# Kernel optimization log

Measured on AMD Instinct MI355X. Metric: run time of the kernel, lower is better.

## Reference

```python
import jax, jax.numpy as jnp
import numpy as np

B = 4096
SEQ = 128            # window_size * rnn_in_pkts
WINDOW = 32
IN_PKTS = 4
LEN_V, LEN_E = 1500, 64
IPD_V, IPD_E = 256, 64
EV = 64              # embedding_vector_bits
RNN_IN = IN_PKTS * EV   # 256
H = 256              # rnn_hidden_bits
LABELS = 100


def setup_inputs() -> dict:
    key = jax.random.key(0)
    ks = jax.random.split(key, 12)
    s = 0.05
    return {
        "len_x": jax.random.randint(ks[0], (B, SEQ), 0, LEN_V),
        "ipd_x": jax.random.randint(ks[1], (B, SEQ), 0, IPD_V),
        "len_emb": jax.random.normal(ks[2], (LEN_V, LEN_E), jnp.float32) * s,
        "ipd_emb": jax.random.normal(ks[3], (IPD_V, IPD_E), jnp.float32) * s,
        "fc_w": jax.random.normal(ks[4], (EV, LEN_E + IPD_E), jnp.float32) * s,
        "fc_b": jax.random.normal(ks[5], (EV,), jnp.float32) * s,
        "w_ih": jax.random.normal(ks[6], (3 * H, RNN_IN), jnp.float32) * s,
        "w_hh": jax.random.normal(ks[7], (3 * H, H), jnp.float32) * s,
        "b_ih": jax.random.normal(ks[8], (3 * H,), jnp.float32) * s,
        "b_hh": jax.random.normal(ks[9], (3 * H,), jnp.float32) * s,
        "out_w": jax.random.normal(ks[10], (LABELS, H), jnp.float32) * s,
        "out_b": jax.random.normal(ks[11], (LABELS,), jnp.float32) * s,
    }


def _gru_scan(rnn_in, w_ih, w_hh, b_ih, b_hh):
    # rnn_in: [B, T, RNN_IN]. Precompute input-side gates for all steps at once.
    gi_all = jnp.einsum("bti,gi->btg", rnn_in, w_ih) + b_ih  # [B,T,3H]
    h0 = jnp.zeros((rnn_in.shape[0], H), rnn_in.dtype)

    def step(h, gi):
        gh = h @ w_hh.T + b_hh                 # [B,3H]
        i_r, i_z, i_n = jnp.split(gi, 3, axis=-1)
        h_r, h_z, h_n = jnp.split(gh, 3, axis=-1)
        r = jax.nn.sigmoid(i_r + h_r)
        z = jax.nn.sigmoid(i_z + h_z)
        n = jnp.tanh(i_n + r * h_n)
        h_new = (1.0 - z) * n + z * h
        return h_new, None

    h_final, _ = jax.lax.scan(step, h0, jnp.swapaxes(gi_all, 0, 1))
    return h_final


def reference(len_x, ipd_x, len_emb, ipd_emb, fc_w, fc_b, w_ih, w_hh, b_ih, b_hh, out_w, out_b):
    len_e = len_emb[len_x]                      # [B,SEQ,LEN_E]
    ipd_e = ipd_emb[ipd_x]                      # [B,SEQ,IPD_E]
    cat = jnp.concatenate([len_e, ipd_e], axis=-1)
    evs = cat @ fc_w.T + fc_b                   # [B,SEQ,EV]
    rnn_in = evs.reshape(B, WINDOW, RNN_IN)     # [B,32,256]
    h = _gru_scan(rnn_in, w_ih, w_hh, b_ih, b_hh)
    logits = h @ out_w.T + out_b                # [B,LABELS]
    return logits
```

## Files before the change

### kernel.cpp

```cpp
#include <hip/hip_runtime.h>
#include <hip/hip_bf16.h>

typedef __bf16 bf16_t;
typedef __bf16 bf16x8 __attribute__((ext_vector_type(8)));
typedef float f32x4 __attribute__((ext_vector_type(4)));
typedef unsigned short u16x4 __attribute__((ext_vector_type(4)));

#define MFMA16(a, b, c) __builtin_amdgcn_mfma_f32_16x16x32_bf16((a), (b), (c), 0, 0, 0)

#define BATCH 4096
#define SEQN 128
#define HN 256
#define NLABELS 100
#define TSTEPS 32
#define LEN_VN 1500
#define IPD_VN 256

#define OFF_LENT   0u
#define OFF_IPDT   384000u
#define OFF_WIH    449536u
#define OFF_WHH    842752u
#define OFF_GI     1235968u

__device__ __forceinline__ float sigf(float x) {
    return __builtin_amdgcn_rcpf(1.f + __expf(-x));
}
__device__ __forceinline__ float tanh_fast(float x) {
    return 2.f * __builtin_amdgcn_rcpf(1.f + __expf(-2.f * x)) - 1.f;
}
__device__ __forceinline__ float b2f(unsigned short v) {
    union { unsigned u; float f; } c; c.u = ((unsigned)v) << 16; return c.f;
}
__device__ __forceinline__ f32x4 b2f4(u16x4 v) {
    f32x4 o;
    #pragma unroll
    for (int r = 0; r < 4; ++r) o[r] = b2f(v[r]);
    return o;
}
__device__ __forceinline__ unsigned short f2b(float f) {
    union { bf16_t h; unsigned short s; } c; c.h = (bf16_t)f; return c.s;
}

__device__ __forceinline__ void barrier_lds() {
    asm volatile("s_waitcnt lgkmcnt(0)\n\ts_barrier" ::: "memory");
}
__device__ __forceinline__ void wait_vm0() {
    asm volatile("s_waitcnt vmcnt(0)" ::: "memory");
}

#define PREP_TBL_BLOCKS 110
__global__ void prep_kernel(const float* __restrict__ len_emb,
                            const float* __restrict__ ipd_emb,
                            const float* __restrict__ fc_w,
                            const float* __restrict__ fc_b,
                            const float* __restrict__ w_ih,
                            const float* __restrict__ w_hh,
                            float* __restrict__ lenT, float* __restrict__ ipdT,
                            bf16_t* __restrict__ wfrag_ih,
                            bf16_t* __restrict__ wfrag_hh) {
    const int bid = blockIdx.x, tid = threadIdx.x;
    if (bid < PREP_TBL_BLOCKS) {
        __shared__ float w_lds[64 * 132];
        __shared__ float emb_lds[16 * 64];
        const int row0 = bid * 16;

        #pragma unroll
        for (int k = 0; k < 8; ++k) {
            const int l = k * 1024 + tid * 4;
            const int e = l >> 7, j = l & 127;
            *(f32x4*)(w_lds + e * 132 + j) = *(const f32x4*)(fc_w + l);
        }
        {
            const int r = tid >> 4;
            const int c = (tid & 15) * 4;
            const int grow = row0 + r;
            f32x4 v = {};
            if (grow < LEN_VN)               v = *(const f32x4*)(len_emb + grow * 64 + c);
            else if (grow < LEN_VN + IPD_VN) v = *(const f32x4*)(ipd_emb + (grow - LEN_VN) * 64 + c);
            *(f32x4*)(emb_lds + r * 64 + c) = v;
        }
        __syncthreads();

        const int e = tid & 63;
        const int r0 = tid >> 6;
        const float* wrow_lo = w_lds + e * 132;
        #pragma unroll
        for (int rr = 0; rr < 4; ++rr) {
            const int r = r0 + rr * 4;
            const int grow = row0 + r;
            if (grow >= LEN_VN + IPD_VN) break;
            const bool is_len = grow < LEN_VN;
            const float* wrow = is_len ? wrow_lo : (wrow_lo + 64);
            f32x4 acc = {};
            #pragma unroll
            for (int c = 0; c < 16; ++c) {
                f32x4 wv = *(const f32x4*)(wrow + c * 4);
                f32x4 ev = *(const f32x4*)(emb_lds + r * 64 + c * 4);
                acc += wv * ev;
            }
            float s = acc[0] + acc[1] + acc[2] + acc[3] + (is_len ? fc_b[e] : 0.f);
            if (is_len) lenT[grow * 64 + e] = s;
            else        ipdT[(grow - LEN_VN) * 64 + e] = s;
        }
    } else {
        const int flat = (bid - PREP_TBL_BLOCKS) * 256 + tid;
        const int which = flat / 24576;
        const int rem = flat % 24576;
        const int c = rem >> 9;
        const int kt = (rem >> 6) & 7;
        const int lane = rem & 63;
        const int g = c * 16 + (lane & 15);
        const int k0 = kt * 32 + (lane >> 4) * 8;
        const float* src = (which == 0 ? w_ih : w_hh) + g * 256 + k0;
        bf16_t* dst = (which == 0 ? wfrag_ih : wfrag_hh) + ((c * 8 + kt) * 64 + lane) * 8;
        f32x4 s0 = *(const f32x4*)(src);
        f32x4 s1 = *(const f32x4*)(src + 4);
        bf16x8 o;
        #pragma unroll
        for (int j = 0; j < 4; ++j) { o[j] = (bf16_t)s0[j]; o[4 + j] = (bf16_t)s1[j]; }
        *(bf16x8*)dst = o;
    }
}

__global__ void __launch_bounds__(1024, 4)
fused_kernel(const int* __restrict__ len_x, const int* __restrict__ ipd_x,
             const float* __restrict__ lenT, const float* __restrict__ ipdT,
             const bf16_t* __restrict__ wfrag_ih,
             const bf16_t* __restrict__ wfrag_hh,
             const float* __restrict__ b_ih, const float* __restrict__ b_hh,
             bf16_t* gi,
             const float* __restrict__ out_w,
             const float* __restrict__ out_b,
             float* __restrict__ out) {
    __shared__ char smem[147456];
    bf16_t* wlds = (bf16_t*)smem;
    bf16_t* dbuf = (bf16_t*)(smem + 131072);
    float* h_fin = (float*)smem;

    const int tid = threadIdx.x;
    const int lane = tid & 63;
    const int w = tid >> 6;
    const int bt = blockIdx.x;
    const int quad = lane >> 4;
    const int b = lane & 15;

    bf16_t* gib = gi + (size_t)bt * 48 * 32 * 256 + lane * 4;
    const bf16_t* wb = &wlds[w * 8 * 512 + lane * 8];

    {
        bf16x8 wri[2][8];
        #pragma unroll
        for (int cc = 0; cc < 2; ++cc) {
            const int ct = cc * 16 + w;
            #pragma unroll
            for (int kt = 0; kt < 8; ++kt)
                wri[cc][kt] = *(const bf16x8*)(wfrag_ih + ((ct * 8 + kt) * 64 + lane) * 8);
        }
        #pragma unroll
        for (int kt = 0; kt < 8; ++kt)
            *(bf16x8*)&wlds[(w * 8 + kt) * 512 + lane * 8] =
                *(const bf16x8*)(wfrag_ih + (((32 + w) * 8 + kt) * 64 + lane) * 8);

        f32x4 bias0 = *(const f32x4*)(b_ih + w * 16 + quad * 4)
                    + *(const f32x4*)(b_hh + w * 16 + quad * 4);
        f32x4 bias1 = *(const f32x4*)(b_ih + 256 + w * 16 + quad * 4)
                    + *(const f32x4*)(b_hh + 256 + w * 16 + quad * 4);
        f32x4 bias2 = *(const f32x4*)(b_ih + 512 + w * 16 + quad * 4);

        const int sub = tid & 511;
        const int pr = sub >> 3;
        const int sub8 = sub & 7;
        const int grow = pr & 15;
        const int p = pr >> 4;
        const int e0 = sub8 * 8;
        const int b_row = bt * 16 + grow;
        const int goff = (2 * p + (sub8 >> 2)) * 512 + ((sub8 & 3) * 16 + grow) * 8;

        auto do_gather = [&](int t) {
            const int seq = t * 4 + p;
            const int v1 = len_x[b_row * SEQN + seq];
            const int v2 = ipd_x[b_row * SEQN + seq];
            const float* lp = lenT + v1 * 64 + e0;
            const float* ip = ipdT + v2 * 64 + e0;
            f32x4 a0 = *(const f32x4*)lp + *(const f32x4*)ip;
            f32x4 a1 = *(const f32x4*)(lp + 4) + *(const f32x4*)(ip + 4);
            bf16x8 o;
            #pragma unroll
            for (int j = 0; j < 4; ++j) { o[j] = (bf16_t)a0[j]; o[4 + j] = (bf16_t)a1[j]; }
            *(bf16x8*)&dbuf[(t & 1) * 4096 + goff] = o;
        };

        if (tid < 512) do_gather(0);

        for (int t = 0; t < TSTEPS; ++t) {
            barrier_lds();
            if (t + 1 < TSTEPS && tid < 512) do_gather(t + 1);

            f32x4 acc0 = bias0, acc1 = bias1, acc2 = bias2;
            const bf16_t* ab = &dbuf[(t & 1) * 4096 + lane * 8];
            #pragma unroll
            for (int kt = 0; kt < 8; ++kt) {
                bf16x8 xf = *(const bf16x8*)(ab + kt * 512);
                bf16x8 w5 = *(const bf16x8*)(wb + kt * 512);
                acc0 = MFMA16(wri[0][kt], xf, acc0);
                acc1 = MFMA16(wri[1][kt], xf, acc1);
                acc2 = MFMA16(w5, xf, acc2);
            }

            u16x4 o0, o1, o2;
            #pragma unroll
            for (int r = 0; r < 4; ++r) {
                o0[r] = f2b(acc0[r]); o1[r] = f2b(acc1[r]); o2[r] = f2b(acc2[r]);
            }
            *(u16x4*)(gib + ((size_t)(w) * 32 + t) * 256) = o0;
            *(u16x4*)(gib + ((size_t)(16 + w) * 32 + t) * 256) = o1;
            *(u16x4*)(gib + ((size_t)(32 + w) * 32 + t) * 256) = o2;
        }
    }

    barrier_lds();
    wait_vm0();

    bf16_t* h_lds = dbuf;

    bf16x8 wr[2][8];
    #pragma unroll
    for (int cc = 0; cc < 2; ++cc) {
        const int ct = cc * 16 + w;
        #pragma unroll
        for (int kt = 0; kt < 8; ++kt)
            wr[cc][kt] = *(const bf16x8*)(wfrag_hh + ((ct * 8 + kt) * 64 + lane) * 8);
    }
    #pragma unroll
    for (int kt = 0; kt < 8; ++kt)
        *(bf16x8*)&wlds[(w * 8 + kt) * 512 + lane * 8] =
            *(const bf16x8*)(wfrag_hh + (((32 + w) * 8 + kt) * 64 + lane) * 8);

    const f32x4 bhn = *(const f32x4*)(b_hh + (32 + w) * 16 + quad * 4);

    for (int i = tid; i < 4096; i += 1024) h_lds[4096 + i] = (bf16_t)0.f;

    const int j0 = 16 * w + 4 * quad;
    const int woff = (j0 >> 5) * 512 + ((((j0 >> 3) & 3)) * 16 + b) * 8 + (j0 & 7);

    u16x4 gc0 = *(const u16x4*)(gib + ((size_t)(w) * 32) * 256);
    u16x4 gc1 = *(const u16x4*)(gib + ((size_t)(16 + w) * 32) * 256);
    u16x4 gc2 = *(const u16x4*)(gib + ((size_t)(32 + w) * 32) * 256);

    f32x4 hprev = {};

    for (int t = 0; t < TSTEPS; ++t) {
        barrier_lds();

        f32x4 acc0 = b2f4(gc0);
        f32x4 acc1 = b2f4(gc1);
        f32x4 acc2 = bhn;
        u16x4 g2cur = gc2;

        if (t + 1 < TSTEPS) {
            gc0 = *(const u16x4*)(gib + ((size_t)(w) * 32 + t + 1) * 256);
            gc1 = *(const u16x4*)(gib + ((size_t)(16 + w) * 32 + t + 1) * 256);
            gc2 = *(const u16x4*)(gib + ((size_t)(32 + w) * 32 + t + 1) * 256);
        }

        const bf16_t* hb = &h_lds[((t + 1) & 1) * 4096 + lane * 8];
        #pragma unroll
        for (int kt = 0; kt < 8; ++kt) {
            bf16x8 hf = *(const bf16x8*)(hb + kt * 512);
            bf16x8 w5 = *(const bf16x8*)(wb + kt * 512);
            acc0 = MFMA16(wr[0][kt], hf, acc0);
            acc1 = MFMA16(wr[1][kt], hf, acc1);
            acc2 = MFMA16(w5, hf, acc2);
        }

        f32x4 rg, zg;
        #pragma unroll
        for (int r = 0; r < 4; ++r) { rg[r] = sigf(acc0[r]); zg[r] = sigf(acc1[r]); }
        f32x4 u = b2f4(g2cur) + rg * acc2;
        f32x4 ng;
        #pragma unroll
        for (int r = 0; r < 4; ++r) ng[r] = tanh_fast(u[r]);
        f32x4 hn = ng + zg * (hprev - ng);
        hprev = hn;

        u16x4 o;
        #pragma unroll
        for (int r = 0; r < 4; ++r) o[r] = f2b(hn[r]);
        *(u16x4*)(&h_lds[(t & 1) * 4096 + woff]) = o;
    }

    __syncthreads();

    *(f32x4*)(h_fin + b * 260 + j0) = hprev;
    __syncthreads();

    for (int i = tid; i < 16 * NLABELS; i += 1024) {
        const int row = i / NLABELS;
        const int cl = i - row * NLABELS;
        const f32x4* wrow = (const f32x4*)(out_w + cl * 256);
        const f32x4* hr = (const f32x4*)(h_fin + row * 260);
        f32x4 acc = {0.f, 0.f, 0.f, 0.f};
        #pragma unroll 4
        for (int k = 0; k < 64; ++k) acc += hr[k] * wrow[k];
        out[(bt * 16 + row) * NLABELS + cl] =
            out_b[cl] + acc[0] + acc[1] + acc[2] + acc[3];
    }
}

extern "C" void kernel_launch(void* const* d_in, const int* in_sizes, int n_in,
                              void* d_out, int out_size, void* d_ws, size_t ws_size,
                              hipStream_t stream) {
    (void)in_sizes; (void)n_in; (void)out_size; (void)ws_size;
    const int*   len_x   = (const int*)d_in[0];
    const int*   ipd_x   = (const int*)d_in[1];
    const float* len_emb = (const float*)d_in[2];
    const float* ipd_emb = (const float*)d_in[3];
    const float* fc_w    = (const float*)d_in[4];
    const float* fc_b    = (const float*)d_in[5];
    const float* w_ih    = (const float*)d_in[6];
    const float* w_hh    = (const float*)d_in[7];
    const float* b_ih    = (const float*)d_in[8];
    const float* b_hh    = (const float*)d_in[9];
    const float* out_w   = (const float*)d_in[10];
    const float* out_b   = (const float*)d_in[11];

    char* ws = (char*)d_ws;
    float*  lenT = (float*)(ws + OFF_LENT);
    float*  ipdT = (float*)(ws + OFF_IPDT);
    bf16_t* wfi  = (bf16_t*)(ws + OFF_WIH);
    bf16_t* wfh  = (bf16_t*)(ws + OFF_WHH);
    bf16_t* gi   = (bf16_t*)(ws + OFF_GI);

    prep_kernel<<<302, 256, 0, stream>>>(len_emb, ipd_emb, fc_w, fc_b,
                                         w_ih, w_hh, lenT, ipdT, wfi, wfh);
    fused_kernel<<<256, 1024, 0, stream>>>(len_x, ipd_x, lenT, ipdT, wfi, wfh,
                                           b_ih, b_hh, gi, out_w, out_b,
                                           (float*)d_out);
}
```

Measured before the change: 228.4 us.

## Interleave input-gate GEMM and GRU recurrence in 8-step chunks

Splits the 32 time steps into four chunks of 8 and alternates, per chunk, between computing input-side gates and running the recurrence. The gi scratch buffer per block shrinks from 32 to 8 steps so it is more likely to stay in cache instead of round-tripping through HBM. In exchange the w_ih and w_hh fragments are reloaded into registers and LDS four times each, and LDS grows to hold separate x and h buffers, which may lower occupancy or add reload latency.

```diff
diff --git a/kernel.cpp b/kernel.cpp
--- a/kernel.cpp
+++ b/kernel.cpp
@@ -15,6 +15,8 @@
 #define TSTEPS 32
 #define LEN_VN 1500
 #define IPD_VN 256
+#define CHUNK 8
+#define NCHUNK 4
 
 #define OFF_LENT   0u
 #define OFF_IPDT   384000u
@@ -132,9 +134,10 @@
              const float* __restrict__ out_w,
              const float* __restrict__ out_b,
              float* __restrict__ out) {
-    __shared__ char smem[147456];
+    __shared__ char smem[163840];
     bf16_t* wlds = (bf16_t*)smem;
-    bf16_t* dbuf = (bf16_t*)(smem + 131072);
+    bf16_t* xbuf = (bf16_t*)(smem + 131072);
+    bf16_t* hbuf = (bf16_t*)(smem + 147456);
     float* h_fin = (float*)smem;
 
     const int tid = threadIdx.x;
@@ -144,66 +147,71 @@
     const int quad = lane >> 4;
     const int b = lane & 15;
 
-    bf16_t* gib = gi + (size_t)bt * 48 * 32 * 256 + lane * 4;
+    bf16_t* gib = gi + (size_t)bt * (48 * CHUNK * 256) + lane * 4;
     const bf16_t* wb = &wlds[w * 8 * 512 + lane * 8];
 
-    {
-        bf16x8 wri[2][8];
-        #pragma unroll
-        for (int cc = 0; cc < 2; ++cc) {
-            const int ct = cc * 16 + w;
-            #pragma unroll
-            for (int kt = 0; kt < 8; ++kt)
-                wri[cc][kt] = *(const bf16x8*)(wfrag_ih + ((ct * 8 + kt) * 64 + lane) * 8);
-        }
-        #pragma unroll
-        for (int kt = 0; kt < 8; ++kt)
+    f32x4 bias0 = *(const f32x4*)(b_ih + w * 16 + quad * 4)
+                + *(const f32x4*)(b_hh + w * 16 + quad * 4);
+    f32x4 bias1 = *(const f32x4*)(b_ih + 256 + w * 16 + quad * 4)
+                + *(const f32x4*)(b_hh + 256 + w * 16 + quad * 4);
+    f32x4 bias2 = *(const f32x4*)(b_ih + 512 + w * 16 + quad * 4);
+    const f32x4 bhn = *(const f32x4*)(b_hh + (32 + w) * 16 + quad * 4);
+
+    const int sub = tid & 511;
+    const int pr = sub >> 3;
+    const int sub8 = sub & 7;
+    const int grow = pr & 15;
+    const int p = pr >> 4;
+    const int e0 = sub8 * 8;
+    const int b_row = bt * 16 + grow;
+    const int goff = (2 * p + (sub8 >> 2)) * 512 + ((sub8 & 3) * 16 + grow) * 8;
+
+    auto do_gather = [&](int t) {
+        const int seq = t * 4 + p;
+        const int v1 = len_x[b_row * SEQN + seq];
+        const int v2 = ipd_x[b_row * SEQN + seq];
+        const float* lp = lenT + v1 * 64 + e0;
+        const float* ip = ipdT + v2 * 64 + e0;
+        f32x4 a0 = *(const f32x4*)lp + *(const f32x4*)ip;
+        f32x4 a1 = *(const f32x4*)(lp + 4) + *(const f32x4*)(ip + 4);
+        bf16x8 o;
+        #pragma unroll
+        for (int j = 0; j < 4; ++j) { o[j] = (bf16_t)a0[j]; o[4 + j] = (bf16_t)a1[j]; }
+        *(bf16x8*)&xbuf[(t & 1) * 4096 + goff] = o;
+    };
+
+    for (int i = tid; i < 4096; i += 1024) hbuf[4096 + i] = (bf16_t)0.f;
+
+    const int j0 = 16 * w + 4 * quad;
+    const int woff = (j0 >> 5) * 512 + (((j0 >> 3) & 3) * 16 + b) * 8 + (j0 & 7);
+
+    if (tid < 512) do_gather(0);
+
+    f32x4 hprev = {};
+    bf16x8 wreg0[8], wreg1[8];
+
+    for (int ck = 0; ck < NCHUNK; ++ck) {
+        #pragma unroll
+        for (int kt = 0; kt < 8; ++kt) {
+            wreg0[kt] = *(const bf16x8*)(wfrag_ih + ((w * 8 + kt) * 64 + lane) * 8);
+            wreg1[kt] = *(const bf16x8*)(wfrag_ih + (((16 + w) * 8 + kt) * 64 + lane) * 8);
             *(bf16x8*)&wlds[(w * 8 + kt) * 512 + lane * 8] =
                 *(const bf16x8*)(wfrag_ih + (((32 + w) * 8 + kt) * 64 + lane) * 8);
-
-        f32x4 bias0 = *(const f32x4*)(b_ih + w * 16 + quad * 4)
-                    + *(const f32x4*)(b_hh + w * 16 + quad * 4);
-        f32x4 bias1 = *(const f32x4*)(b_ih + 256 + w * 16 + quad * 4)
-                    + *(const f32x4*)(b_hh + 256 + w * 16 + quad * 4);
-        f32x4 bias2 = *(const f32x4*)(b_ih + 512 + w * 16 + quad * 4);
-
-        const int sub = tid & 511;
-        const int pr = sub >> 3;
-        const int sub8 = sub & 7;
-        const int grow = pr & 15;
-        const int p = pr >> 4;
-        const int e0 = sub8 * 8;
-        const int b_row = bt * 16 + grow;
-        const int goff = (2 * p + (sub8 >> 2)) * 512 + ((sub8 & 3) * 16 + grow) * 8;
-
-        auto do_gather = [&](int t) {
-            const int seq = t * 4 + p;
-            const int v1 = len_x[b_row * SEQN + seq];
-            const int v2 = ipd_x[b_row * SEQN + seq];
-            const float* lp = lenT + v1 * 64 + e0;
-            const float* ip = ipdT + v2 * 64 + e0;
-            f32x4 a0 = *(const f32x4*)lp + *(const f32x4*)ip;
-            f32x4 a1 = *(const f32x4*)(lp + 4) + *(const f32x4*)(ip + 4);
-            bf16x8 o;
-            #pragma unroll
-            for (int j = 0; j < 4; ++j) { o[j] = (bf16_t)a0[j]; o[4 + j] = (bf16_t)a1[j]; }
-            *(bf16x8*)&dbuf[(t & 1) * 4096 + goff] = o;
-        };
-
-        if (tid < 512) do_gather(0);
-
-        for (int t = 0; t < TSTEPS; ++t) {
+        }
+
+        for (int tc = 0; tc < CHUNK; ++tc) {
+            const int t = ck * CHUNK + tc;
             barrier_lds();
             if (t + 1 < TSTEPS && tid < 512) do_gather(t + 1);
 
             f32x4 acc0 = bias0, acc1 = bias1, acc2 = bias2;
-            const bf16_t* ab = &dbuf[(t & 1) * 4096 + lane * 8];
+            const bf16_t* ab = &xbuf[(t & 1) * 4096 + lane * 8];
             #pragma unroll
             for (int kt = 0; kt < 8; ++kt) {
                 bf16x8 xf = *(const bf16x8*)(ab + kt * 512);
                 bf16x8 w5 = *(const bf16x8*)(wb + kt * 512);
-                acc0 = MFMA16(wri[0][kt], xf, acc0);
-                acc1 = MFMA16(wri[1][kt], xf, acc1);
+                acc0 = MFMA16(wreg0[kt], xf, acc0);
+                acc1 = MFMA16(wreg1[kt], xf, acc1);
                 acc2 = MFMA16(w5, xf, acc2);
             }
 
@@ -212,81 +220,65 @@
             for (int r = 0; r < 4; ++r) {
                 o0[r] = f2b(acc0[r]); o1[r] = f2b(acc1[r]); o2[r] = f2b(acc2[r]);
             }
-            *(u16x4*)(gib + ((size_t)(w) * 32 + t) * 256) = o0;
-            *(u16x4*)(gib + ((size_t)(16 + w) * 32 + t) * 256) = o1;
-            *(u16x4*)(gib + ((size_t)(32 + w) * 32 + t) * 256) = o2;
-        }
-    }
-
-    barrier_lds();
-    wait_vm0();
-
-    bf16_t* h_lds = dbuf;
-
-    bf16x8 wr[2][8];
-    #pragma unroll
-    for (int cc = 0; cc < 2; ++cc) {
-        const int ct = cc * 16 + w;
-        #pragma unroll
-        for (int kt = 0; kt < 8; ++kt)
-            wr[cc][kt] = *(const bf16x8*)(wfrag_hh + ((ct * 8 + kt) * 64 + lane) * 8);
-    }
-    #pragma unroll
-    for (int kt = 0; kt < 8; ++kt)
-        *(bf16x8*)&wlds[(w * 8 + kt) * 512 + lane * 8] =
-            *(const bf16x8*)(wfrag_hh + (((32 + w) * 8 + kt) * 64 + lane) * 8);
-
-    const f32x4 bhn = *(const f32x4*)(b_hh + (32 + w) * 16 + quad * 4);
-
-    for (int i = tid; i < 4096; i += 1024) h_lds[4096 + i] = (bf16_t)0.f;
-
-    const int j0 = 16 * w + 4 * quad;
-    const int woff = (j0 >> 5) * 512 + ((((j0 >> 3) & 3)) * 16 + b) * 8 + (j0 & 7);
-
-    u16x4 gc0 = *(const u16x4*)(gib + ((size_t)(w) * 32) * 256);
-    u16x4 gc1 = *(const u16x4*)(gib + ((size_t)(16 + w) * 32) * 256);
-    u16x4 gc2 = *(const u16x4*)(gib + ((size_t)(32 + w) * 32) * 256);
-
-    f32x4 hprev = {};
-
-    for (int t = 0; t < TSTEPS; ++t) {
-        barrier_lds();
-
-        f32x4 acc0 = b2f4(gc0);
-        f32x4 acc1 = b2f4(gc1);
-        f32x4 acc2 = bhn;
-        u16x4 g2cur = gc2;
-
-        if (t + 1 < TSTEPS) {
-            gc0 = *(const u16x4*)(gib + ((size_t)(w) * 32 + t + 1) * 256);
-            gc1 = *(const u16x4*)(gib + ((size_t)(16 + w) * 32 + t + 1) * 256);
-            gc2 = *(const u16x4*)(gib + ((size_t)(32 + w) * 32 + t + 1) * 256);
-        }
-
-        const bf16_t* hb = &h_lds[((t + 1) & 1) * 4096 + lane * 8];
+            *(u16x4*)(gib + ((w) * CHUNK + tc) * 256) = o0;
+            *(u16x4*)(gib + ((16 + w) * CHUNK + tc) * 256) = o1;
+            *(u16x4*)(gib + ((32 + w) * CHUNK + tc) * 256) = o2;
+        }
+
+        wait_vm0();
+
+        u16x4 gc0 = *(const u16x4*)(gib + ((w) * CHUNK) * 256);
+        u16x4 gc1 = *(const u16x4*)(gib + ((16 + w) * CHUNK) * 256);
+        u16x4 gc2 = *(const u16x4*)(gib + ((32 + w) * CHUNK) * 256);
+
         #pragma unroll
         for (int kt = 0; kt < 8; ++kt) {
-            bf16x8 hf = *(const bf16x8*)(hb + kt * 512);
-            bf16x8 w5 = *(const bf16x8*)(wb + kt * 512);
-            acc0 = MFMA16(wr[0][kt], hf, acc0);
-            acc1 = MFMA16(wr[1][kt], hf, acc1);
-            acc2 = MFMA16(w5, hf, acc2);
-        }
-
-        f32x4 rg, zg;
-        #pragma unroll
-        for (int r = 0; r < 4; ++r) { rg[r] = sigf(acc0[r]); zg[r] = sigf(acc1[r]); }
-        f32x4 u = b2f4(g2cur) + rg * acc2;
-        f32x4 ng;
-        #pragma unroll
-        for (int r = 0; r < 4; ++r) ng[r] = tanh_fast(u[r]);
-        f32x4 hn = ng + zg * (hprev - ng);
-        hprev = hn;
-
-        u16x4 o;
-        #pragma unroll
-        for (int r = 0; r < 4; ++r) o[r] = f2b(hn[r]);
-        *(u16x4*)(&h_lds[(t & 1) * 4096 + woff]) = o;
+            wreg0[kt] = *(const bf16x8*)(wfrag_hh + ((w * 8 + kt) * 64 + lane) * 8);
+            wreg1[kt] = *(const bf16x8*)(wfrag_hh + (((16 + w) * 8 + kt) * 64 + lane) * 8);
+            *(bf16x8*)&wlds[(w * 8 + kt) * 512 + lane * 8] =
+                *(const bf16x8*)(wfrag_hh + (((32 + w) * 8 + kt) * 64 + lane) * 8);
+        }
+
+        for (int tc = 0; tc < CHUNK; ++tc) {
+            const int t = ck * CHUNK + tc;
+            barrier_lds();
+
+            f32x4 acc0 = b2f4(gc0);
+            f32x4 acc1 = b2f4(gc1);
+            f32x4 acc2 = bhn;
+            u16x4 g2cur = gc2;
+
+            if (tc + 1 < CHUNK) {
+                gc0 = *(const u16x4*)(gib + ((w) * CHUNK + tc + 1) * 256);
+                gc1 = *(const u16x4*)(gib + ((16 + w) * CHUNK + tc + 1) * 256);
+                gc2 = *(const u16x4*)(gib + ((32 + w) * CHUNK + tc + 1) * 256);
+            }
+
+            const bf16_t* hb = &hbuf[((t + 1) & 1) * 4096 + lane * 8];
+            #pragma unroll
+            for (int kt = 0; kt < 8; ++kt) {
+                bf16x8 hf = *(const bf16x8*)(hb + kt * 512);
+                bf16x8 w5 = *(const bf16x8*)(wb + kt * 512);
+                acc0 = MFMA16(wreg0[kt], hf, acc0);
+                acc1 = MFMA16(wreg1[kt], hf, acc1);
+                acc2 = MFMA16(w5, hf, acc2);
+            }
+
+            f32x4 rg, zg;
+            #pragma unroll
+            for (int r = 0; r < 4; ++r) { rg[r] = sigf(acc0[r]); zg[r] = sigf(acc1[r]); }
+            f32x4 u = b2f4(g2cur) + rg * acc2;
+            f32x4 ng;
+            #pragma unroll
+            for (int r = 0; r < 4; ++r) ng[r] = tanh_fast(u[r]);
+            f32x4 hn = ng + zg * (hprev - ng);
+            hprev = hn;
+
+            u16x4 o;
+            #pragma unroll
+            for (int r = 0; r < 4; ++r) o[r] = f2b(hn[r]);
+            *(u16x4*)(&hbuf[(t & 1) * 4096 + woff]) = o;
+        }
     }
 
     __syncthreads();
```

After: 379.6 us. +66.2%, slower.
